# Optimization experiments

Measured on AMD Instinct MI355X. Metric: run time of the kernel, lower is better.

Reference implementation:

```python
import jax, jax.numpy as jnp
import numpy as np

NUM_LAYERS = 3  # min_num_layers == max_num_layers == 3 (deterministic stochastic depth)
LN_EPS = 1e-5


def setup_inputs() -> dict:
    key = jax.random.key(0)
    k1, k2, k3 = jax.random.split(key, 3)
    N, d, F = 8, 16, 512  # (batch, in_dim=out_dim, num_features)
    x = jax.random.normal(k1, (N, d, F), dtype=jnp.float32)
    W = jax.random.normal(k2, (d, F, F, d), dtype=jnp.float32)  # recurrent weight
    A = jax.random.uniform(k3, (2, F, F), dtype=jnp.float32)    # transition mats, steps 1..2
    return {"x": x, "W": W, "A": A}


def _contract(h, W, a):
    # h: (N,d,F), W: (d,F,F,o), a: (F,F) -> (N,o,F)
    # Equivalent to (h.unsqueeze(-1).unsqueeze(-1) * (W * a[...,None])).sum(1).sum(1).transpose(1,2)
    return jnp.einsum('ndf,dfgo,fg->nog', h, W, a)


def _layer_norm(y):
    # torch applies layer_norm over the channel dim (axis 1 of (N,o,F)), no affine params
    m = y.mean(axis=1, keepdims=True)
    v = y.var(axis=1, keepdims=True)
    return (y - m) / jnp.sqrt(v + LN_EPS)


def reference(x, W, A):
    history = [x]
    for i in range(1, NUM_LAYERS):
        # recurrent + residual branch: average contributions from all previous layers
        ys = [_contract(history[j], W, A[i - j - 1]) for j in range(i)]
        y = jnp.mean(jnp.stack(ys, axis=0), axis=0)
        y = _layer_norm(y)
        history.append(y)
    return history[-1]  # return_layers='last'
```

## Files before the change

### kernel.cpp

```cpp
#include <hip/hip_runtime.h>
#include <stdint.h>


#define FC   32
#define NCH  16

typedef _Float16 h8 __attribute__((ext_vector_type(8)));

__global__ __launch_bounds__(256)
void k_pass_a(const float* __restrict__ W, const float* __restrict__ A,
              const float* __restrict__ x,
              float* __restrict__ p0, float* __restrict__ p1,
              _Float16* __restrict__ Wh) {
    __shared__ float sx[FC][16][8];
    __shared__ float sA0[FC][16];
    __shared__ float sA1[FC][16];

    const int t  = threadIdx.x;
    const int fc = blockIdx.x;
    const int ct = blockIdx.y;
    const int f0 = fc * FC;

#pragma unroll
    for (int k = 0; k < 16; ++k) {
        int idx = k * 256 + t;
        int fl = idx >> 7, d = (idx >> 3) & 15, n = idx & 7;
        sx[fl][d][n] = x[n * 8192 + d * 512 + f0 + fl];
    }
#pragma unroll
    for (int k = 0; k < 2; ++k) {
        int idx = k * 256 + t;
        int fl = idx >> 4, gl = idx & 15;
        sA0[fl][gl] = A[(size_t)(f0 + fl) * 512 + ct * 16 + gl];
        sA1[fl][gl] = A[262144 + (size_t)(f0 + fl) * 512 + ct * 16 + gl];
    }
    __syncthreads();

    const int gl  = t >> 4;
    const int o   = t & 15;
    const int col = (ct * 16 + gl) * 16 + o;
    const float* Wc = W + col;

    float c0[8], c1[8];
#pragma unroll
    for (int n = 0; n < 8; ++n) { c0[n] = 0.f; c1[n] = 0.f; }

    for (int fl = 0; fl < FC; ++fl) {
        const int f = f0 + fl;
        float w[16];
#pragma unroll
        for (int d = 0; d < 16; ++d)
            w[d] = Wc[(size_t)d * 4194304 + (size_t)f * 8192];

        {
            h8 lo, hi;
#pragma unroll
            for (int d = 0; d < 8; ++d) { lo[d] = (_Float16)w[d]; hi[d] = (_Float16)w[d + 8]; }
            h8* wp = reinterpret_cast<h8*>(Wh + ((size_t)f * 8192 + col) * 16);
            wp[0] = lo;
            wp[1] = hi;
        }

        float p[8];
#pragma unroll
        for (int n = 0; n < 8; ++n) p[n] = 0.f;
#pragma unroll
        for (int d = 0; d < 16; ++d) {
            float4 xa = *reinterpret_cast<const float4*>(&sx[fl][d][0]);
            float4 xb = *reinterpret_cast<const float4*>(&sx[fl][d][4]);
            p[0] = fmaf(xa.x, w[d], p[0]);
            p[1] = fmaf(xa.y, w[d], p[1]);
            p[2] = fmaf(xa.z, w[d], p[2]);
            p[3] = fmaf(xa.w, w[d], p[3]);
            p[4] = fmaf(xb.x, w[d], p[4]);
            p[5] = fmaf(xb.y, w[d], p[5]);
            p[6] = fmaf(xb.z, w[d], p[6]);
            p[7] = fmaf(xb.w, w[d], p[7]);
        }

        const float a0 = sA0[fl][gl];
        const float a1 = sA1[fl][gl];
#pragma unroll
        for (int n = 0; n < 8; ++n) {
            c0[n] = fmaf(a0, p[n], c0[n]);
            c1[n] = fmaf(a1, p[n], c1[n]);
        }
    }

    size_t base = ((size_t)fc * 8192 + col) * 8;
    float4* dst0 = reinterpret_cast<float4*>(p0 + base);
    dst0[0] = make_float4(c0[0], c0[1], c0[2], c0[3]);
    dst0[1] = make_float4(c0[4], c0[5], c0[6], c0[7]);
    float4* dst1 = reinterpret_cast<float4*>(p1 + base);
    dst1[0] = make_float4(c1[0], c1[1], c1[2], c1[3]);
    dst1[1] = make_float4(c1[4], c1[5], c1[6], c1[7]);
}

__global__ __launch_bounds__(256)
void k_pass_b(const _Float16* __restrict__ Wh, const float* __restrict__ A,
              const float* __restrict__ c0p, float* __restrict__ p2) {
    __shared__ float sx[FC][16][8];
    __shared__ float sA0[FC][16];

    const int t  = threadIdx.x;
    const int fc = blockIdx.x;
    const int ct = blockIdx.y;
    const int f0 = fc * FC;

#pragma unroll
    for (int k = 0; k < 16; ++k) {
        int idx = k * 256 + t;
        int fl = idx >> 7, o = (idx >> 3) & 15, n = idx & 7;
        float s = 0.f;
#pragma unroll
        for (int ch = 0; ch < NCH; ++ch)
            s += c0p[(((size_t)ch * 512 + f0 + fl) * 16 + o) * 8 + n];
        sx[fl][o][n] = s;
    }
    __syncthreads();
    {
        int fl = t >> 3, n = t & 7;
        float m = 0.f, v = 0.f;
#pragma unroll
        for (int oo = 0; oo < 16; ++oo) { float y = sx[fl][oo][n]; m += y; v += y * y; }
        m *= (1.f / 16.f);
        v = v * (1.f / 16.f) - m * m;
        float r = rsqrtf(v + 1e-5f);
#pragma unroll
        for (int oo = 0; oo < 16; ++oo) sx[fl][oo][n] = (sx[fl][oo][n] - m) * r;
    }
#pragma unroll
    for (int k = 0; k < 2; ++k) {
        int idx = k * 256 + t;
        int fl = idx >> 4, gl = idx & 15;
        sA0[fl][gl] = A[(size_t)(f0 + fl) * 512 + ct * 16 + gl];
    }
    __syncthreads();

    const int gl  = t >> 4;
    const int col = ct * 256 + t;

    float c2[8];
#pragma unroll
    for (int n = 0; n < 8; ++n) c2[n] = 0.f;

    for (int fl = 0; fl < FC; ++fl) {
        const int f = f0 + fl;
        const h8* wp = reinterpret_cast<const h8*>(Wh + ((size_t)f * 8192 + col) * 16);
        h8 lo = wp[0];
        h8 hi = wp[1];
        float w[16];
#pragma unroll
        for (int d = 0; d < 8; ++d) { w[d] = (float)lo[d]; w[d + 8] = (float)hi[d]; }

        float p[8];
#pragma unroll
        for (int n = 0; n < 8; ++n) p[n] = 0.f;
#pragma unroll
        for (int d = 0; d < 16; ++d) {
            float4 xa = *reinterpret_cast<const float4*>(&sx[fl][d][0]);
            float4 xb = *reinterpret_cast<const float4*>(&sx[fl][d][4]);
            p[0] = fmaf(xa.x, w[d], p[0]);
            p[1] = fmaf(xa.y, w[d], p[1]);
            p[2] = fmaf(xa.z, w[d], p[2]);
            p[3] = fmaf(xa.w, w[d], p[3]);
            p[4] = fmaf(xb.x, w[d], p[4]);
            p[5] = fmaf(xb.y, w[d], p[5]);
            p[6] = fmaf(xb.z, w[d], p[6]);
            p[7] = fmaf(xb.w, w[d], p[7]);
        }

        const float a0 = sA0[fl][gl];
#pragma unroll
        for (int n = 0; n < 8; ++n) c2[n] = fmaf(a0, p[n], c2[n]);
    }

    size_t base = ((size_t)fc * 8192 + col) * 8;
    float4* dst = reinterpret_cast<float4*>(p2 + base);
    dst[0] = make_float4(c2[0], c2[1], c2[2], c2[3]);
    dst[1] = make_float4(c2[4], c2[5], c2[6], c2[7]);
}

__global__ __launch_bounds__(128)
void k_final(const float* __restrict__ p1, const float* __restrict__ p2,
             float* __restrict__ out) {
    __shared__ float sh[16][8];
    int g = blockIdx.x;
    int t = threadIdx.x;
    int o = t >> 3, n = t & 7;
    float s0 = 0.f, s1 = 0.f;
#pragma unroll
    for (int ch = 0; ch < NCH; ++ch) {
        size_t idx = (((size_t)ch * 512 + g) * 16 + o) * 8 + n;
        s0 += p1[idx];
        s1 += p2[idx];
    }
    float s = 0.5f * (s0 + s1);
    sh[o][n] = s;
    __syncthreads();
    float m = 0.f, v = 0.f;
#pragma unroll
    for (int oo = 0; oo < 16; ++oo) { float y = sh[oo][n]; m += y; v += y * y; }
    m *= (1.f / 16.f);
    v = v * (1.f / 16.f) - m * m;
    float r = rsqrtf(v + 1e-5f);
    out[n * 8192 + o * 512 + g] = (s - m) * r;
}

extern "C" void kernel_launch(void* const* d_in, const int* in_sizes, int n_in,
                              void* d_out, int out_size, void* d_ws, size_t ws_size,
                              hipStream_t stream) {
    const float* x = (const float*)d_in[0];
    const float* W = (const float*)d_in[1];
    const float* A = (const float*)d_in[2];
    float* out = (float*)d_out;

    float* ws  = (float*)d_ws;
    float* c0p = ws;
    float* c1p = c0p + 1048576;
    float* c2p = c1p + 1048576;
    _Float16* Wh = (_Float16*)(c2p + 1048576);

    k_pass_a<<<dim3(NCH, 32), 256, 0, stream>>>(W, A, x, c0p, c1p, Wh);
    k_pass_b<<<dim3(NCH, 32), 256, 0, stream>>>(Wh, A, c0p, c2p);
    k_final<<<512, 128, 0, stream>>>(c1p, c2p, out);
}
```

Before: 422.7 us.

## Fuse the three passes into one kernel with grid barriers and drop the fp16 weight copy

```diff
diff --git a/kernel.cpp b/kernel.cpp
--- a/kernel.cpp
+++ b/kernel.cpp
@@ -4,14 +4,14 @@
 
 #define FC   32
 #define NCH  16
-
-typedef _Float16 h8 __attribute__((ext_vector_type(8)));
+#define NBLK 512u
 
 __global__ __launch_bounds__(256)
-void k_pass_a(const float* __restrict__ W, const float* __restrict__ A,
-              const float* __restrict__ x,
-              float* __restrict__ p0, float* __restrict__ p1,
-              _Float16* __restrict__ Wh) {
+void k_fused(const float* __restrict__ W, const float* __restrict__ A,
+             const float* __restrict__ x,
+             float* __restrict__ c0p, float* __restrict__ c1p,
+             float* __restrict__ c2p, float* __restrict__ out,
+             unsigned* __restrict__ bar) {
     __shared__ float sx[FC][16][8];
     __shared__ float sA0[FC][16];
     __shared__ float sA1[FC][16];
@@ -37,75 +37,62 @@
     __syncthreads();
 
     const int gl  = t >> 4;
-    const int o   = t & 15;
-    const int col = (ct * 16 + gl) * 16 + o;
+    const int col = ct * 256 + t;
     const float* Wc = W + col;
 
-    float c0[8], c1[8];
-#pragma unroll
-    for (int n = 0; n < 8; ++n) { c0[n] = 0.f; c1[n] = 0.f; }
-
-    for (int fl = 0; fl < FC; ++fl) {
-        const int f = f0 + fl;
-        float w[16];
-#pragma unroll
-        for (int d = 0; d < 16; ++d)
-            w[d] = Wc[(size_t)d * 4194304 + (size_t)f * 8192];
-
-        {
-            h8 lo, hi;
-#pragma unroll
-            for (int d = 0; d < 8; ++d) { lo[d] = (_Float16)w[d]; hi[d] = (_Float16)w[d + 8]; }
-            h8* wp = reinterpret_cast<h8*>(Wh + ((size_t)f * 8192 + col) * 16);
-            wp[0] = lo;
-            wp[1] = hi;
+    {
+        float c0[8], c1[8];
+#pragma unroll
+        for (int n = 0; n < 8; ++n) { c0[n] = 0.f; c1[n] = 0.f; }
+
+        for (int fl = 0; fl < FC; ++fl) {
+            const int f = f0 + fl;
+            float w[16];
+#pragma unroll
+            for (int d = 0; d < 16; ++d)
+                w[d] = Wc[(size_t)d * 4194304 + (size_t)f * 8192];
+
+            float p[8];
+#pragma unroll
+            for (int n = 0; n < 8; ++n) p[n] = 0.f;
+#pragma unroll
+            for (int d = 0; d < 16; ++d) {
+                float4 xa = *reinterpret_cast<const float4*>(&sx[fl][d][0]);
+                float4 xb = *reinterpret_cast<const float4*>(&sx[fl][d][4]);
+                p[0] = fmaf(xa.x, w[d], p[0]);
+                p[1] = fmaf(xa.y, w[d], p[1]);
+                p[2] = fmaf(xa.z, w[d], p[2]);
+                p[3] = fmaf(xa.w, w[d], p[3]);
+                p[4] = fmaf(xb.x, w[d], p[4]);
+                p[5] = fmaf(xb.y, w[d], p[5]);
+                p[6] = fmaf(xb.z, w[d], p[6]);
+                p[7] = fmaf(xb.w, w[d], p[7]);
+            }
+            const float a0 = sA0[fl][gl];
+            const float a1 = sA1[fl][gl];
+#pragma unroll
+            for (int n = 0; n < 8; ++n) {
+                c0[n] = fmaf(a0, p[n], c0[n]);
+                c1[n] = fmaf(a1, p[n], c1[n]);
+            }
         }
-
-        float p[8];
-#pragma unroll
-        for (int n = 0; n < 8; ++n) p[n] = 0.f;
-#pragma unroll
-        for (int d = 0; d < 16; ++d) {
-            float4 xa = *reinterpret_cast<const float4*>(&sx[fl][d][0]);
-            float4 xb = *reinterpret_cast<const float4*>(&sx[fl][d][4]);
-            p[0] = fmaf(xa.x, w[d], p[0]);
-            p[1] = fmaf(xa.y, w[d], p[1]);
-            p[2] = fmaf(xa.z, w[d], p[2]);
-            p[3] = fmaf(xa.w, w[d], p[3]);
-            p[4] = fmaf(xb.x, w[d], p[4]);
-            p[5] = fmaf(xb.y, w[d], p[5]);
-            p[6] = fmaf(xb.z, w[d], p[6]);
-            p[7] = fmaf(xb.w, w[d], p[7]);
-        }
-
-        const float a0 = sA0[fl][gl];
-        const float a1 = sA1[fl][gl];
-#pragma unroll
-        for (int n = 0; n < 8; ++n) {
-            c0[n] = fmaf(a0, p[n], c0[n]);
-            c1[n] = fmaf(a1, p[n], c1[n]);
-        }
-    }
-
-    size_t base = ((size_t)fc * 8192 + col) * 8;
-    float4* dst0 = reinterpret_cast<float4*>(p0 + base);
-    dst0[0] = make_float4(c0[0], c0[1], c0[2], c0[3]);
-    dst0[1] = make_float4(c0[4], c0[5], c0[6], c0[7]);
-    float4* dst1 = reinterpret_cast<float4*>(p1 + base);
-    dst1[0] = make_float4(c1[0], c1[1], c1[2], c1[3]);
-    dst1[1] = make_float4(c1[4], c1[5], c1[6], c1[7]);
-}
-
-__global__ __launch_bounds__(256)
-void k_pass_b(const _Float16* __restrict__ Wh, const float* __restrict__ A,
-              const float* __restrict__ c0p, float* __restrict__ p2) {
-    __shared__ float sx[FC][16][8];
-    __shared__ float sA0[FC][16];
-
-    const int t  = threadIdx.x;
-    const int fc = blockIdx.x;
-    const int ct = blockIdx.y;
-    const int f0 = fc * FC;
+        size_t base = ((size_t)fc * 8192 + col) * 8;
+        float4* dst0 = reinterpret_cast<float4*>(c0p + base);
+        dst0[0] = make_float4(c0[0], c0[1], c0[2], c0[3]);
+        dst0[1] = make_float4(c0[4], c0[5], c0[6], c0[7]);
+        float4* dst1 = reinterpret_cast<float4*>(c1p + base);
+        dst1[0] = make_float4(c1[0], c1[1], c1[2], c1[3]);
+        dst1[1] = make_float4(c1[4], c1[5], c1[6], c1[7]);
+    }
+
+    __threadfence();
+    __syncthreads();
+    if (t == 0) {
+        atomicAdd(&bar[0], 1u);
+        while (atomicAdd(&bar[0], 0u) < NBLK) __builtin_amdgcn_s_sleep(2);
+    }
+    __syncthreads();
+    __threadfence();
 
 #pragma unroll
     for (int k = 0; k < 16; ++k) {
@@ -129,82 +116,82 @@
 #pragma unroll
         for (int oo = 0; oo < 16; ++oo) sx[fl][oo][n] = (sx[fl][oo][n] - m) * r;
     }
-#pragma unroll
-    for (int k = 0; k < 2; ++k) {
-        int idx = k * 256 + t;
-        int fl = idx >> 4, gl = idx & 15;
-        sA0[fl][gl] = A[(size_t)(f0 + fl) * 512 + ct * 16 + gl];
-    }
-    __syncthreads();
-
-    const int gl  = t >> 4;
-    const int col = ct * 256 + t;
-
-    float c2[8];
-#pragma unroll
-    for (int n = 0; n < 8; ++n) c2[n] = 0.f;
-
-    for (int fl = 0; fl < FC; ++fl) {
-        const int f = f0 + fl;
-        const h8* wp = reinterpret_cast<const h8*>(Wh + ((size_t)f * 8192 + col) * 16);
-        h8 lo = wp[0];
-        h8 hi = wp[1];
-        float w[16];
-#pragma unroll
-        for (int d = 0; d < 8; ++d) { w[d] = (float)lo[d]; w[d + 8] = (float)hi[d]; }
-
-        float p[8];
-#pragma unroll
-        for (int n = 0; n < 8; ++n) p[n] = 0.f;
-#pragma unroll
-        for (int d = 0; d < 16; ++d) {
-            float4 xa = *reinterpret_cast<const float4*>(&sx[fl][d][0]);
-            float4 xb = *reinterpret_cast<const float4*>(&sx[fl][d][4]);
-            p[0] = fmaf(xa.x, w[d], p[0]);
-            p[1] = fmaf(xa.y, w[d], p[1]);
-            p[2] = fmaf(xa.z, w[d], p[2]);
-            p[3] = fmaf(xa.w, w[d], p[3]);
-            p[4] = fmaf(xb.x, w[d], p[4]);
-            p[5] = fmaf(xb.y, w[d], p[5]);
-            p[6] = fmaf(xb.z, w[d], p[6]);
-            p[7] = fmaf(xb.w, w[d], p[7]);
+    __syncthreads();
+
+    {
+        float c2[8];
+#pragma unroll
+        for (int n = 0; n < 8; ++n) c2[n] = 0.f;
+
+        for (int s = 0; s < FC; ++s) {
+            const int fl = FC - 1 - s;
+            const int f  = f0 + fl;
+            float w[16];
+#pragma unroll
+            for (int d = 0; d < 16; ++d)
+                w[d] = Wc[(size_t)d * 4194304 + (size_t)f * 8192];
+
+            float p[8];
+#pragma unroll
+            for (int n = 0; n < 8; ++n) p[n] = 0.f;
+#pragma unroll
+            for (int d = 0; d < 16; ++d) {
+                float4 xa = *reinterpret_cast<const float4*>(&sx[fl][d][0]);
+                float4 xb = *reinterpret_cast<const float4*>(&sx[fl][d][4]);
+                p[0] = fmaf(xa.x, w[d], p[0]);
+                p[1] = fmaf(xa.y, w[d], p[1]);
+                p[2] = fmaf(xa.z, w[d], p[2]);
+                p[3] = fmaf(xa.w, w[d], p[3]);
+                p[4] = fmaf(xb.x, w[d], p[4]);
+                p[5] = fmaf(xb.y, w[d], p[5]);
+                p[6] = fmaf(xb.z, w[d], p[6]);
+                p[7] = fmaf(xb.w, w[d], p[7]);
+            }
+            const float a0 = sA0[fl][gl];
+#pragma unroll
+            for (int n = 0; n < 8; ++n) c2[n] = fmaf(a0, p[n], c2[n]);
         }
-
-        const float a0 = sA0[fl][gl];
-#pragma unroll
-        for (int n = 0; n < 8; ++n) c2[n] = fmaf(a0, p[n], c2[n]);
-    }
-
-    size_t base = ((size_t)fc * 8192 + col) * 8;
-    float4* dst = reinterpret_cast<float4*>(p2 + base);
-    dst[0] = make_float4(c2[0], c2[1], c2[2], c2[3]);
-    dst[1] = make_float4(c2[4], c2[5], c2[6], c2[7]);
-}
-
-__global__ __launch_bounds__(128)
-void k_final(const float* __restrict__ p1, const float* __restrict__ p2,
-             float* __restrict__ out) {
-    __shared__ float sh[16][8];
-    int g = blockIdx.x;
-    int t = threadIdx.x;
-    int o = t >> 3, n = t & 7;
-    float s0 = 0.f, s1 = 0.f;
-#pragma unroll
-    for (int ch = 0; ch < NCH; ++ch) {
-        size_t idx = (((size_t)ch * 512 + g) * 16 + o) * 8 + n;
-        s0 += p1[idx];
-        s1 += p2[idx];
-    }
-    float s = 0.5f * (s0 + s1);
-    sh[o][n] = s;
-    __syncthreads();
-    float m = 0.f, v = 0.f;
-#pragma unroll
-    for (int oo = 0; oo < 16; ++oo) { float y = sh[oo][n]; m += y; v += y * y; }
-    m *= (1.f / 16.f);
-    v = v * (1.f / 16.f) - m * m;
-    float r = rsqrtf(v + 1e-5f);
-    out[n * 8192 + o * 512 + g] = (s - m) * r;
+        size_t base = ((size_t)fc * 8192 + col) * 8;
+        float4* dst = reinterpret_cast<float4*>(c2p + base);
+        dst[0] = make_float4(c2[0], c2[1], c2[2], c2[3]);
+        dst[1] = make_float4(c2[4], c2[5], c2[6], c2[7]);
+    }
+
+    __threadfence();
+    __syncthreads();
+    if (t == 0) {
+        atomicAdd(&bar[1], 1u);
+        while (atomicAdd(&bar[1], 0u) < NBLK) __builtin_amdgcn_s_sleep(2);
+    }
+    __syncthreads();
+    __threadfence();
+
+    float* sh = &sA0[0][0];
+    const int g = fc * 32 + ct;
+    float sval = 0.f;
+    if (t < 128) {
+        int o = t >> 3, n = t & 7;
+        float s0 = 0.f, s1 = 0.f;
+#pragma unroll
+        for (int ch = 0; ch < NCH; ++ch) {
+            size_t idx = (((size_t)ch * 512 + g) * 16 + o) * 8 + n;
+            s0 += c1p[idx];
+            s1 += c2p[idx];
+        }
+        sval = 0.5f * (s0 + s1);
+        sh[o * 8 + n] = sval;
+    }
+    __syncthreads();
+    if (t < 128) {
+        int o = t >> 3, n = t & 7;
+        float m = 0.f, v = 0.f;
+#pragma unroll
+        for (int oo = 0; oo < 16; ++oo) { float y = sh[oo * 8 + n]; m += y; v += y * y; }
+        m *= (1.f / 16.f);
+        v = v * (1.f / 16.f) - m * m;
+        float r = rsqrtf(v + 1e-5f);
+        out[n * 8192 + o * 512 + g] = (sval - m) * r;
+    }
 }
 
 extern "C" void kernel_launch(void* const* d_in, const int* in_sizes, int n_in,
@@ -216,12 +203,11 @@
     float* out = (float*)d_out;
 
     float* ws  = (float*)d_ws;
-    float* c0p = ws;
+    unsigned* bar = (unsigned*)d_ws;
+    float* c0p = ws + 256;
     float* c1p = c0p + 1048576;
     float* c2p = c1p + 1048576;
-    _Float16* Wh = (_Float16*)(c2p + 1048576);
-
-    k_pass_a<<<dim3(NCH, 32), 256, 0, stream>>>(W, A, x, c0p, c1p, Wh);
-    k_pass_b<<<dim3(NCH, 32), 256, 0, stream>>>(Wh, A, c0p, c2p);
-    k_final<<<512, 128, 0, stream>>>(c1p, c2p, out);
+
+    hipMemsetAsync(d_ws, 0, 2 * sizeof(unsigned), stream);
+    k_fused<<<dim3(NCH, 32), 256, 0, stream>>>(W, A, x, c0p, c1p, c2p, out, bar);
 }
```

Result: slower. 690.7 us (+63.4%).
